# Kernel tuning notes

Measured on AMD Instinct MI355X. Metric: run time of the kernel, lower is better.

The kernel has to match this reference:

```python
import jax, jax.numpy as jnp
import numpy as np

B, S, IN_DIM, HID = 128, 512, 512, 1024


def setup_inputs() -> dict:
    key = jax.random.key(0)
    k0, k1, k2, k3, k4 = jax.random.split(key, 5)
    s_ih = 1.0 / np.sqrt(HID)
    return {
        "embedding_sequence": jax.random.normal(k0, (B, S, IN_DIM), dtype=jnp.float32),
        "w_ih": jax.random.uniform(k1, (3 * HID, IN_DIM), jnp.float32, -s_ih, s_ih),
        "w_hh": jax.random.uniform(k2, (3 * HID, HID), jnp.float32, -s_ih, s_ih),
        "b_ih": jax.random.uniform(k3, (3 * HID,), jnp.float32, -s_ih, s_ih),
        "b_hh": jax.random.uniform(k4, (3 * HID,), jnp.float32, -s_ih, s_ih),
    }


def _gru_scan(embedding_sequence, w_ih, w_hh, b_ih, b_hh):
    # Precompute input-side gate projections for all steps: [B,S,3H]
    gi_all = jnp.einsum('bsi,gi->bsg', embedding_sequence, w_ih) + b_ih

    def step(h, gi):
        gh = h @ w_hh.T + b_hh                      # [B,3H]
        i_r, i_z, i_n = jnp.split(gi, 3, axis=-1)
        h_r, h_z, h_n = jnp.split(gh, 3, axis=-1)
        r = jax.nn.sigmoid(i_r + h_r)
        z = jax.nn.sigmoid(i_z + h_z)
        n = jnp.tanh(i_n + r * h_n)
        h_new = (1.0 - z) * n + z * h
        return h_new, h_new

    h0 = jnp.zeros((embedding_sequence.shape[0], HID), dtype=embedding_sequence.dtype)
    h_last, hiddens = jax.lax.scan(step, h0, jnp.swapaxes(gi_all, 0, 1))
    return jnp.swapaxes(hiddens, 0, 1), h_last      # ([B,S,H], [B,H])


def reference(embedding_sequence, w_ih, w_hh, b_ih, b_hh):
    return _gru_scan(embedding_sequence, w_ih, w_hh, b_ih, b_hh)
```

## Files before the change

kernel.cpp:

```cpp
#include <hip/hip_runtime.h>
#include <hip/hip_bf16.h>

#define BB   128
#define SS   512
#define IND  512
#define HID  1024
#define NBLK 256
#define GRPBLK 64
#define NSTRIPE 8

typedef __attribute__((ext_vector_type(8))) short s8v;
typedef __attribute__((ext_vector_type(4))) float f4v;
typedef unsigned long long u64;
typedef unsigned int u32;

__device__ __forceinline__ short f2bf(float f) {
    union { float f; u32 u; } v; v.f = f;
    u32 u = v.u + 0x7FFFu + ((v.u >> 16) & 1u);
    return (short)(u >> 16);
}


__global__ void __launch_bounds__(128, 1)
gru_persistent(const float* __restrict__ X,
               const float* __restrict__ Wih,
               const float* __restrict__ Whh,
               const float* __restrict__ bih,
               const float* __restrict__ bhh,
               float* __restrict__ out,
               short* __restrict__ bufA,
               short* __restrict__ bufB,
               u64*   __restrict__ ctr)
{
    __shared__ __align__(16) short whh2[32 * 3 * 64 * 8];
    __shared__ __align__(16) short wih2[16 * 3 * 64 * 8];

    const int tid  = threadIdx.x;
    const int wave = tid >> 6;
    const int lane = tid & 63;
    const int blk  = blockIdx.x;
    const int mi   = blk >> 6;
    const int jg   = blk & 63;

    for (int idx = tid; idx < 48 * (HID / 4); idx += 128) {
        int s = idx >> 8, k4 = idx & 255;
        int g = s >> 4, n_ = s & 15;
        int grow = g * HID + jg * 16 + n_;
        float4 v = *(const float4*)(Whh + (size_t)grow * HID + k4 * 4);
        int k  = k4 * 4;
        int kk = k >> 5, kg_ = (k >> 3) & 3, e0 = k & 7;
        short* d = &whh2[((((kk * 3 + g) << 6) | (kg_ * 16 + n_)) << 3) + e0];
        d[0] = f2bf(v.x); d[1] = f2bf(v.y); d[2] = f2bf(v.z); d[3] = f2bf(v.w);
    }
    for (int idx = tid; idx < 48 * (IND / 4); idx += 128) {
        int s = idx >> 7, k4 = idx & 127;
        int g = s >> 4, n_ = s & 15;
        int grow = g * HID + jg * 16 + n_;
        float4 v = *(const float4*)(Wih + (size_t)grow * IND + k4 * 4);
        int k  = k4 * 4;
        int kk = k >> 5, kg_ = (k >> 3) & 3, e0 = k & 7;
        short* d = &wih2[((((kk * 3 + g) << 6) | (kg_ * 16 + n_)) << 3) + e0];
        d[0] = f2bf(v.x); d[1] = f2bf(v.y); d[2] = f2bf(v.z); d[3] = f2bf(v.w);
    }

    const int n  = lane & 15;
    const int kg = lane >> 4;
    const int j  = jg * 16 + n;
    const float bir = bih[j], biz = bih[HID + j], bin_ = bih[2 * HID + j];
    const float bhr = bhh[j], bhz = bhh[HID + j], bhn  = bhh[2 * HID + j];

    const int rowbase = mi * 32 + wave * 16;
    const int wg      = mi * 2 + wave;

    const int wkk = j >> 5, wkg = (j >> 3) & 3;
    const u32 rest   = (u32)wkk * 1024u + (u32)wkg * 256u
                     + (u32)kg * 64u + ((u32)(n & 7) << 1);
    const u32 wbyteA = (u32)wg * 32768u + rest;
    const u32 wbyteB = (u32)mi * 131072u + (u32)(wg & 1) * 32768u + rest;

    const u64* hbA = (const u64*)bufA + (size_t)wg * 4096 + lane * 2;
    const u64* hbB = (const u64*)bufB + (size_t)mi * 16384
                   + (size_t)(wg & 1) * 4096 + lane * 2;

    float hkeep[4] = {0.f, 0.f, 0.f, 0.f};

    __syncthreads();

    for (int t = 0; t < SS; ++t) {
        f4v acc_r  = {0.f,0.f,0.f,0.f};
        f4v acc_z  = {0.f,0.f,0.f,0.f};
        f4v acc_in = {0.f,0.f,0.f,0.f};
        f4v acc_hn = {0.f,0.f,0.f,0.f};

        {
            const float* xrow = X + ((size_t)(rowbase + n) * SS + t) * IND;
            #pragma unroll 4
            for (int kk = 0; kk < IND / 32; ++kk) {
                const int k0 = kk * 32 + kg * 8;
                const float4* px = (const float4*)(xrow + k0);
                float4 x0 = px[0], x1 = px[1];
                s8v a;
                a[0]=f2bf(x0.x); a[1]=f2bf(x0.y); a[2]=f2bf(x0.z); a[3]=f2bf(x0.w);
                a[4]=f2bf(x1.x); a[5]=f2bf(x1.y); a[6]=f2bf(x1.z); a[7]=f2bf(x1.w);
                s8v br = *(const s8v*)&wih2[(((kk * 3 + 0) << 6) | lane) << 3];
                s8v bz = *(const s8v*)&wih2[(((kk * 3 + 1) << 6) | lane) << 3];
                s8v bn = *(const s8v*)&wih2[(((kk * 3 + 2) << 6) | lane) << 3];
                acc_r  = __builtin_amdgcn_mfma_f32_16x16x32_bf16(a, br, acc_r,  0,0,0);
                acc_z  = __builtin_amdgcn_mfma_f32_16x16x32_bf16(a, bz, acc_z,  0,0,0);
                acc_in = __builtin_amdgcn_mfma_f32_16x16x32_bf16(a, bn, acc_in, 0,0,0);
            }
        }

        if (t > 0) {
            const u64* hb = (t & 1) ? hbA : hbB;
            s8v areg[32];
            #pragma unroll
            for (int kk = 0; kk < 32; ++kk) {
                u64 lo = __hip_atomic_load(hb + kk * 128,
                                           __ATOMIC_RELAXED, __HIP_MEMORY_SCOPE_AGENT);
                u64 hi = __hip_atomic_load(hb + kk * 128 + 1,
                                           __ATOMIC_RELAXED, __HIP_MEMORY_SCOPE_AGENT);
                union { u64 q[2]; s8v v; } u; u.q[0] = lo; u.q[1] = hi;
                areg[kk] = u.v;
            }
            #pragma unroll
            for (int kk = 0; kk < 32; ++kk) {
                s8v br = *(const s8v*)&whh2[(((kk * 3 + 0) << 6) | lane) << 3];
                s8v bz = *(const s8v*)&whh2[(((kk * 3 + 1) << 6) | lane) << 3];
                s8v bn = *(const s8v*)&whh2[(((kk * 3 + 2) << 6) | lane) << 3];
                acc_r  = __builtin_amdgcn_mfma_f32_16x16x32_bf16(areg[kk], br, acc_r,  0,0,0);
                acc_z  = __builtin_amdgcn_mfma_f32_16x16x32_bf16(areg[kk], bz, acc_z,  0,0,0);
                acc_hn = __builtin_amdgcn_mfma_f32_16x16x32_bf16(areg[kk], bn, acc_hn, 0,0,0);
            }
        }

        u32 packv[4];
        #pragma unroll
        for (int r = 0; r < 4; ++r) {
            const int b = rowbase + kg * 4 + r;
            float gr = acc_r[r] + bir + bhr;
            float gz = acc_z[r] + biz + bhz;
            float rr = 1.f / (1.f + __expf(-gr));
            float zz = 1.f / (1.f + __expf(-gz));
            float hn = acc_hn[r] + bhn;
            float na = acc_in[r] + bin_ + rr * hn;
            float e2 = __expf(2.f * na);
            float nn = (e2 - 1.f) / (e2 + 1.f);
            float hnew = (1.f - zz) * nn + zz * hkeep[r];
            hkeep[r] = hnew;
            out[(size_t)b * (SS * HID) + (size_t)t * HID + j] = hnew;
            if (t == SS - 1)
                out[(size_t)BB * SS * HID + (size_t)b * HID + j] = hnew;
            u32 hb16  = (u32)(unsigned short)f2bf(hnew);
            u32 other = (u32)__shfl_xor((int)hb16, 1);
            packv[r] = hb16 | (other << 16);
        }

        if (t < SS - 1) {
            if (!(n & 1)) {
                char* base = (t & 1) ? ((char*)bufB + wbyteB) : ((char*)bufA + wbyteA);
                #pragma unroll
                for (int r = 0; r < 4; ++r)
                    __hip_atomic_store((u32*)(base + r * 16), packv[r],
                                       __ATOMIC_RELAXED, __HIP_MEMORY_SCOPE_AGENT);
            }
            __syncthreads();
            if (tid == 0) {
                __hip_atomic_fetch_add(&ctr[(mi * NSTRIPE + (blk & 7)) * 8], 1ull,
                                       __ATOMIC_RELAXED, __HIP_MEMORY_SCOPE_AGENT);
                const u64 target = (u64)GRPBLK * (u64)(t + 1);
                for (;;) {
                    u64 s = 0;
                    #pragma unroll
                    for (int i = 0; i < NSTRIPE; ++i)
                        s += __hip_atomic_load(&ctr[(mi * NSTRIPE + i) * 8],
                                               __ATOMIC_RELAXED,
                                               __HIP_MEMORY_SCOPE_AGENT);
                    if (s >= target) break;
                    __builtin_amdgcn_s_sleep(1);
                }
            }
            __syncthreads();
        }
    }
}

extern "C" void kernel_launch(void* const* d_in, const int* in_sizes, int n_in,
                              void* d_out, int out_size, void* d_ws, size_t ws_size,
                              hipStream_t stream) {
    const float* X   = (const float*)d_in[0];
    const float* Wih = (const float*)d_in[1];
    const float* Whh = (const float*)d_in[2];
    const float* bih = (const float*)d_in[3];
    const float* bhh = (const float*)d_in[4];
    float* out = (float*)d_out;

    u64*   ctr  = (u64*)d_ws;
    short* bufA = (short*)((char*)d_ws + 4096);
    short* bufB = (short*)(out + (size_t)BB * SS * HID);

    hipMemsetAsync(d_ws, 0, 4096, stream);

    void* args[] = { (void*)&X, (void*)&Wih, (void*)&Whh, (void*)&bih,
                     (void*)&bhh, (void*)&out, (void*)&bufA, (void*)&bufB,
                     (void*)&ctr };
    hipLaunchCooperativeKernel((const void*)gru_persistent,
                               dim3(NBLK), dim3(128), args, 0, stream);
}
```

Baseline: 4.190 ms.

## Issue recurrent hidden-state loads before input projection to overlap latency

Hidden-state loads for the recurrent GEMM are moved ahead of the input-projection MFMA loop and issued as 32 inline-asm dwordx4 loads with sc0 sc1 cache-bypass bits. Their latency can then hide behind the X-side compute, and an explicit waitcnt follows. The LDS weight layout is also reorganised gate-major, with per-gate base pointers, to simplify addressing. The inline asm depends on the scheduler not reordering around it, and it replaces agent-scope atomic loads with cache-bypass flags, which needs correct coherence semantics.

```diff
diff --git a/kernel.cpp b/kernel.cpp
--- a/kernel.cpp
+++ b/kernel.cpp
@@ -32,8 +32,8 @@
                short* __restrict__ bufB,
                u64*   __restrict__ ctr)
 {
-    __shared__ __align__(16) short whh2[32 * 3 * 64 * 8];
-    __shared__ __align__(16) short wih2[16 * 3 * 64 * 8];
+    __shared__ __align__(16) short whh2[3 * 32 * 64 * 8];
+    __shared__ __align__(16) short wih2[3 * 16 * 64 * 8];
 
     const int tid  = threadIdx.x;
     const int wave = tid >> 6;
@@ -49,7 +49,7 @@
         float4 v = *(const float4*)(Whh + (size_t)grow * HID + k4 * 4);
         int k  = k4 * 4;
         int kk = k >> 5, kg_ = (k >> 3) & 3, e0 = k & 7;
-        short* d = &whh2[((((kk * 3 + g) << 6) | (kg_ * 16 + n_)) << 3) + e0];
+        short* d = &whh2[(((g * 32 + kk) * 64) + (kg_ * 16 + n_)) * 8 + e0];
         d[0] = f2bf(v.x); d[1] = f2bf(v.y); d[2] = f2bf(v.z); d[3] = f2bf(v.w);
     }
     for (int idx = tid; idx < 48 * (IND / 4); idx += 128) {
@@ -59,9 +59,16 @@
         float4 v = *(const float4*)(Wih + (size_t)grow * IND + k4 * 4);
         int k  = k4 * 4;
         int kk = k >> 5, kg_ = (k >> 3) & 3, e0 = k & 7;
-        short* d = &wih2[((((kk * 3 + g) << 6) | (kg_ * 16 + n_)) << 3) + e0];
+        short* d = &wih2[(((g * 16 + kk) * 64) + (kg_ * 16 + n_)) * 8 + e0];
         d[0] = f2bf(v.x); d[1] = f2bf(v.y); d[2] = f2bf(v.z); d[3] = f2bf(v.w);
     }
+
+    const short* wihr = wih2;
+    const short* wihz = wih2 + 16 * 64 * 8;
+    const short* wihn = wih2 + 2 * 16 * 64 * 8;
+    const short* whhr = whh2;
+    const short* whhz = whh2 + 32 * 64 * 8;
+    const short* whhn = whh2 + 2 * 32 * 64 * 8;
 
     const int n  = lane & 15;
     const int kg = lane >> 4;
@@ -78,9 +85,9 @@
     const u32 wbyteA = (u32)wg * 32768u + rest;
     const u32 wbyteB = (u32)mi * 131072u + (u32)(wg & 1) * 32768u + rest;
 
-    const u64* hbA = (const u64*)bufA + (size_t)wg * 4096 + lane * 2;
-    const u64* hbB = (const u64*)bufB + (size_t)mi * 16384
-                   + (size_t)(wg & 1) * 4096 + lane * 2;
+    const char* hslabA = (const char*)bufA + (size_t)wg * 32768;
+    const char* hslabB = (const char*)bufB + (size_t)mi * 131072
+                       + (size_t)(wg & 1) * 32768;
 
     float hkeep[4] = {0.f, 0.f, 0.f, 0.f};
 
@@ -91,6 +98,59 @@
         f4v acc_z  = {0.f,0.f,0.f,0.f};
         f4v acc_in = {0.f,0.f,0.f,0.f};
         f4v acc_hn = {0.f,0.f,0.f,0.f};
+        s8v areg[32];
+
+        if (t > 0) {
+            const char* hbase = (t & 1) ? hslabA : hslabB;
+            u64 ha0 = (u64)hbase + (u32)(lane * 16);
+            u64 ha1 = ha0 + 4096,  ha2 = ha0 + 8192,  ha3 = ha0 + 12288;
+            u64 ha4 = ha0 + 16384, ha5 = ha0 + 20480, ha6 = ha0 + 24576;
+            u64 ha7 = ha0 + 28672;
+            asm volatile(
+                "global_load_dwordx4 %0,  %32, off sc0 sc1\n\t"
+                "global_load_dwordx4 %1,  %32, off offset:1024 sc0 sc1\n\t"
+                "global_load_dwordx4 %2,  %32, off offset:2048 sc0 sc1\n\t"
+                "global_load_dwordx4 %3,  %32, off offset:3072 sc0 sc1\n\t"
+                "global_load_dwordx4 %4,  %33, off sc0 sc1\n\t"
+                "global_load_dwordx4 %5,  %33, off offset:1024 sc0 sc1\n\t"
+                "global_load_dwordx4 %6,  %33, off offset:2048 sc0 sc1\n\t"
+                "global_load_dwordx4 %7,  %33, off offset:3072 sc0 sc1\n\t"
+                "global_load_dwordx4 %8,  %34, off sc0 sc1\n\t"
+                "global_load_dwordx4 %9,  %34, off offset:1024 sc0 sc1\n\t"
+                "global_load_dwordx4 %10, %34, off offset:2048 sc0 sc1\n\t"
+                "global_load_dwordx4 %11, %34, off offset:3072 sc0 sc1\n\t"
+                "global_load_dwordx4 %12, %35, off sc0 sc1\n\t"
+                "global_load_dwordx4 %13, %35, off offset:1024 sc0 sc1\n\t"
+                "global_load_dwordx4 %14, %35, off offset:2048 sc0 sc1\n\t"
+                "global_load_dwordx4 %15, %35, off offset:3072 sc0 sc1\n\t"
+                "global_load_dwordx4 %16, %36, off sc0 sc1\n\t"
+                "global_load_dwordx4 %17, %36, off offset:1024 sc0 sc1\n\t"
+                "global_load_dwordx4 %18, %36, off offset:2048 sc0 sc1\n\t"
+                "global_load_dwordx4 %19, %36, off offset:3072 sc0 sc1\n\t"
+                "global_load_dwordx4 %20, %37, off sc0 sc1\n\t"
+                "global_load_dwordx4 %21, %37, off offset:1024 sc0 sc1\n\t"
+                "global_load_dwordx4 %22, %37, off offset:2048 sc0 sc1\n\t"
+                "global_load_dwordx4 %23, %37, off offset:3072 sc0 sc1\n\t"
+                "global_load_dwordx4 %24, %38, off sc0 sc1\n\t"
+                "global_load_dwordx4 %25, %38, off offset:1024 sc0 sc1\n\t"
+                "global_load_dwordx4 %26, %38, off offset:2048 sc0 sc1\n\t"
+                "global_load_dwordx4 %27, %38, off offset:3072 sc0 sc1\n\t"
+                "global_load_dwordx4 %28, %39, off sc0 sc1\n\t"
+                "global_load_dwordx4 %29, %39, off offset:1024 sc0 sc1\n\t"
+                "global_load_dwordx4 %30, %39, off offset:2048 sc0 sc1\n\t"
+                "global_load_dwordx4 %31, %39, off offset:3072 sc0 sc1"
+                : "=&v"(areg[0]),  "=&v"(areg[1]),  "=&v"(areg[2]),  "=&v"(areg[3]),
+                  "=&v"(areg[4]),  "=&v"(areg[5]),  "=&v"(areg[6]),  "=&v"(areg[7]),
+                  "=&v"(areg[8]),  "=&v"(areg[9]),  "=&v"(areg[10]), "=&v"(areg[11]),
+                  "=&v"(areg[12]), "=&v"(areg[13]), "=&v"(areg[14]), "=&v"(areg[15]),
+                  "=&v"(areg[16]), "=&v"(areg[17]), "=&v"(areg[18]), "=&v"(areg[19]),
+                  "=&v"(areg[20]), "=&v"(areg[21]), "=&v"(areg[22]), "=&v"(areg[23]),
+                  "=&v"(areg[24]), "=&v"(areg[25]), "=&v"(areg[26]), "=&v"(areg[27]),
+                  "=&v"(areg[28]), "=&v"(areg[29]), "=&v"(areg[30]), "=&v"(areg[31])
+                : "v"(ha0), "v"(ha1), "v"(ha2), "v"(ha3),
+                  "v"(ha4), "v"(ha5), "v"(ha6), "v"(ha7)
+                : "memory");
+        }
 
         {
             const float* xrow = X + ((size_t)(rowbase + n) * SS + t) * IND;
@@ -102,9 +162,9 @@
                 s8v a;
                 a[0]=f2bf(x0.x); a[1]=f2bf(x0.y); a[2]=f2bf(x0.z); a[3]=f2bf(x0.w);
                 a[4]=f2bf(x1.x); a[5]=f2bf(x1.y); a[6]=f2bf(x1.z); a[7]=f2bf(x1.w);
-                s8v br = *(const s8v*)&wih2[(((kk * 3 + 0) << 6) | lane) << 3];
-                s8v bz = *(const s8v*)&wih2[(((kk * 3 + 1) << 6) | lane) << 3];
-                s8v bn = *(const s8v*)&wih2[(((kk * 3 + 2) << 6) | lane) << 3];
+                s8v br = *(const s8v*)&wihr[((kk << 6) | lane) << 3];
+                s8v bz = *(const s8v*)&wihz[((kk << 6) | lane) << 3];
+                s8v bn = *(const s8v*)&wihn[((kk << 6) | lane) << 3];
                 acc_r  = __builtin_amdgcn_mfma_f32_16x16x32_bf16(a, br, acc_r,  0,0,0);
                 acc_z  = __builtin_amdgcn_mfma_f32_16x16x32_bf16(a, bz, acc_z,  0,0,0);
                 acc_in = __builtin_amdgcn_mfma_f32_16x16x32_bf16(a, bn, acc_in, 0,0,0);
@@ -112,22 +172,13 @@
         }
 
         if (t > 0) {
-            const u64* hb = (t & 1) ? hbA : hbB;
-            s8v areg[32];
+            asm volatile("s_waitcnt vmcnt(0)" ::: "memory");
+            __builtin_amdgcn_sched_barrier(0);
             #pragma unroll
             for (int kk = 0; kk < 32; ++kk) {
-                u64 lo = __hip_atomic_load(hb + kk * 128,
-                                           __ATOMIC_RELAXED, __HIP_MEMORY_SCOPE_AGENT);
-                u64 hi = __hip_atomic_load(hb + kk * 128 + 1,
-                                           __ATOMIC_RELAXED, __HIP_MEMORY_SCOPE_AGENT);
-                union { u64 q[2]; s8v v; } u; u.q[0] = lo; u.q[1] = hi;
-                areg[kk] = u.v;
-            }
-            #pragma unroll
-            for (int kk = 0; kk < 32; ++kk) {
-                s8v br = *(const s8v*)&whh2[(((kk * 3 + 0) << 6) | lane) << 3];
-                s8v bz = *(const s8v*)&whh2[(((kk * 3 + 1) << 6) | lane) << 3];
-                s8v bn = *(const s8v*)&whh2[(((kk * 3 + 2) << 6) | lane) << 3];
+                s8v br = *(const s8v*)&whhr[((kk << 6) | lane) << 3];
+                s8v bz = *(const s8v*)&whhz[((kk << 6) | lane) << 3];
+                s8v bn = *(const s8v*)&whhn[((kk << 6) | lane) << 3];
                 acc_r  = __builtin_amdgcn_mfma_f32_16x16x32_bf16(areg[kk], br, acc_r,  0,0,0);
                 acc_z  = __builtin_amdgcn_mfma_f32_16x16x32_bf16(areg[kk], bz, acc_z,  0,0,0);
                 acc_hn = __builtin_amdgcn_mfma_f32_16x16x32_bf16(areg[kk], bn, acc_hn, 0,0,0);
```

Result: slower. 6.665 ms, median of 2 (+59.1%).
